# Kernel optimization log

Measured on AMD Instinct MI355X. Metric: run time of the kernel, lower is better.

The kernel has to match this reference:

```python
import jax, jax.numpy as jnp
import numpy as np

K_NEIGHBORS = 32  # nsample

def setup_inputs() -> dict:
    key = jax.random.key(0)
    ks = jax.random.split(key, 16)
    B, C, N = 4, 3, 4096
    def w(k, shape):
        return jax.random.normal(k, shape, dtype=jnp.float32) * 0.05
    inp = {"x": jax.random.normal(ks[0], (B, C, N), dtype=jnp.float32)}
    # three scale MLPs share shapes -> stack along leading scale axis (s=3)
    inp["sW0"] = w(ks[1], (3, 64, 3));    inp["sb0"] = w(ks[2], (3, 64))
    inp["sW1"] = w(ks[3], (3, 64, 64));   inp["sb1"] = w(ks[4], (3, 64))
    inp["sW2"] = w(ks[5], (3, 128, 64));  inp["sb2"] = w(ks[6], (3, 128))
    inp["gW0"] = w(ks[7], (256, 384));    inp["gb0"] = w(ks[8], (256,))
    inp["gW1"] = w(ks[9], (1024, 256));   inp["gb1"] = w(ks[10], (1024,))
    inp["mW0"] = w(ks[11], (256, 1024));  inp["mb0"] = w(ks[12], (256,))
    inp["mW1"] = w(ks[13], (128, 256));   inp["mb1"] = w(ks[14], (128,))
    return inp

def _knn_idx(x, k):
    # x: [B, 3, N] channels-first points; k nearest neighbors excluding self
    pts = jnp.swapaxes(x, 1, 2)                       # [B, N, 3]
    sq = jnp.sum(pts * pts, axis=-1)                  # [B, N]
    d = sq[:, :, None] + sq[:, None, :] - 2.0 * jnp.einsum('bnc,bmc->bnm', pts, pts)
    _, idx = jax.lax.top_k(-d, k + 1)                 # nearest first (self at 0)
    return idx[:, :, 1:]                              # [B, N, k]

def reference(x, sW0, sb0, sW1, sb1, sW2, sb2, gW0, gb0, gW1, gb1, mW0, mb0, mW1, mb1):
    B, C, N = x.shape
    # radius is unused by sample_and_group_knn -> all three scales share knn idx
    idx = _knn_idx(x, K_NEIGHBORS)                    # [B, N, K]
    # gather: per-batch x[:, idx[b]] -> [B, C, N, K]
    g = jax.vmap(lambda xf, i: xf[:, i])(x, idx)
    # three shared-weight 1x1-conv MLPs, batched over scale axis s
    h = jax.nn.relu(jnp.einsum('bcnk,soc->sbonk', g, sW0) + sb0[:, None, :, None, None])
    h = jax.nn.relu(jnp.einsum('sbcnk,soc->sbonk', h, sW1) + sb1[:, None, :, None, None])
    h = jax.nn.relu(jnp.einsum('sbcnk,soc->sbonk', h, sW2) + sb2[:, None, :, None, None])
    p = jnp.max(h, axis=-1)                           # [3, B, 128, N] max over neighbors
    point = jnp.moveaxis(p, 0, 1).reshape(B, 3 * p.shape[2], N)  # concat scales -> [B, 384, N]
    gf = jax.nn.relu(jnp.einsum('bcn,oc->bon', point, gW0) + gb0[None, :, None])
    gf = jax.nn.relu(jnp.einsum('bcn,oc->bon', gf, gW1) + gb1[None, :, None])     # [B,1024,N]
    msf = jax.nn.relu(jnp.einsum('bcn,oc->bon', gf, mW0) + mb0[None, :, None])
    msf = jax.nn.relu(jnp.einsum('bcn,oc->bon', msf, mW1) + mb1[None, :, None])   # [B,128,N]
    global_feature = jnp.max(gf, axis=-1)             # [B, 1024]
    return (global_feature, msf)
```

## Files before the change

### kernel.cpp

```cpp
#include <hip/hip_runtime.h>
#include <hip/hip_bf16.h>

#define NPTS 4096
#define KNN  32

typedef __attribute__((ext_vector_type(8))) short short8;
typedef __attribute__((ext_vector_type(4))) float floatx4;
typedef unsigned short u16x2 __attribute__((ext_vector_type(2)));

__device__ __forceinline__ unsigned short f2bf(float f) {
    unsigned u = __float_as_uint(f);
    u = (u + 0x7FFFu + ((u >> 16) & 1u)) >> 16;
    return (unsigned short)u;
}

__global__ __launch_bounds__(256) void prep_all(
    const float* __restrict__ x, float4* __restrict__ pts4,
    const float* __restrict__ gW0, const float* __restrict__ gW1,
    const float* __restrict__ mW0, const float* __restrict__ mW1,
    const float* __restrict__ sW1, const float* __restrict__ sW2,
    unsigned short* __restrict__ Wb0, unsigned short* __restrict__ Wb1,
    unsigned short* __restrict__ Wb2, unsigned short* __restrict__ Wb3,
    unsigned short* __restrict__ Wb4, unsigned short* __restrict__ Wb5)
{
    const int blk = blockIdx.x, t = threadIdx.x;
    if (blk < 64) {
        const int i = blk * 256 + t;
        const int b = i >> 12, n = i & (NPTS - 1);
        const float* xb = x + (size_t)b * 3 * NPTS;
        const float qx = xb[n], qy = xb[NPTS + n], qz = xb[2 * NPTS + n];
        pts4[i] = make_float4(qx, qy, qz, qx * qx + qy * qy + qz * qz);
    } else {
        const int wi = (blk - 64) * 256 + t;
        float v; unsigned short* dst;
        if (wi < 98304)       { v = gW0[wi];          dst = Wb0 + wi; }
        else if (wi < 360448) { v = gW1[wi - 98304];  dst = Wb1 + (wi - 98304); }
        else if (wi < 622592) { v = mW0[wi - 360448]; dst = Wb2 + (wi - 360448); }
        else if (wi < 655360) { v = mW1[wi - 622592]; dst = Wb3 + (wi - 622592); }
        else if (wi < 667648) { v = sW1[wi - 655360]; dst = Wb4 + (wi - 655360); }
        else                  { v = sW2[wi - 667648]; dst = Wb5 + (wi - 667648); }
        *dst = f2bf(v);
    }
}

__global__ __launch_bounds__(256) void knn_kernel16(const float4* __restrict__ pts4,
                                                    int* __restrict__ knn_out)
{
    __shared__ unsigned sred[2][4];
    __shared__ unsigned minS[256];
    __shared__ unsigned long long C[256];
    __shared__ unsigned ccnt;

    const int t = threadIdx.x, wid = t >> 6, lane = t & 63;
    const int q = blockIdx.x, b = q >> 12, n = q & (NPTS - 1);
    const float4* P = pts4 + ((size_t)b << 12);
    const float4 s = P[n];
    const float px = s.x, py = s.y, pz = s.z, sqn = s.w;

    if (t == 0) ccnt = 0u;

    unsigned key[16];
    #pragma unroll
    for (int g = 0; g < 4; ++g) {
        float4 c0 = P[((g * 4 + 0) << 8) + t];
        float4 c1 = P[((g * 4 + 1) << 8) + t];
        float4 c2 = P[((g * 4 + 2) << 8) + t];
        float4 c3 = P[((g * 4 + 3) << 8) + t];
        float d0 = (sqn + c0.w) - 2.0f * (px * c0.x + py * c0.y + pz * c0.z);
        float d1 = (sqn + c1.w) - 2.0f * (px * c1.x + py * c1.y + pz * c1.z);
        float d2 = (sqn + c2.w) - 2.0f * (px * c2.x + py * c2.y + pz * c2.z);
        float d3 = (sqn + c3.w) - 2.0f * (px * c3.x + py * c3.y + pz * c3.z);
        unsigned u0 = __float_as_uint(d0), u1 = __float_as_uint(d1);
        unsigned u2 = __float_as_uint(d2), u3 = __float_as_uint(d3);
        key[g * 4 + 0] = (u0 & 0x80000000u) ? ~u0 : (u0 | 0x80000000u);
        key[g * 4 + 1] = (u1 & 0x80000000u) ? ~u1 : (u1 | 0x80000000u);
        key[g * 4 + 2] = (u2 & 0x80000000u) ? ~u2 : (u2 | 0x80000000u);
        key[g * 4 + 3] = (u3 & 0x80000000u) ? ~u3 : (u3 | 0x80000000u);
    }

    unsigned tm = key[0];
    #pragma unroll
    for (int r = 1; r < 16; ++r) tm = (key[r] < tm) ? key[r] : tm;
    minS[t] = tm;
    __syncthreads();

    unsigned m0 = minS[lane];
    unsigned m1 = minS[lane + 64];
    unsigned m2 = minS[lane + 128];
    unsigned m3 = minS[lane + 192];
    m0 = (m1 < m0) ? m1 : m0;
    m2 = (m3 < m2) ? m3 : m2;
    m0 = (m2 < m0) ? m2 : m0;

    unsigned lo = 0u, hi = 0xFFFFFFFFu;
    for (int i = 0; i < 32; ++i) {
        const unsigned mid = lo + ((hi - lo) >> 1);
        const unsigned cnt = (unsigned)__popcll(__ballot(m0 <= mid));
        if (cnt >= 33u) hi = mid; else lo = mid + 1u;
    }
    const unsigned thr0 = hi;

    #pragma unroll
    for (int r = 0; r < 16; ++r) {
        if (key[r] <= thr0) {
            unsigned p = atomicAdd(&ccnt, 1u);
            if (p < 256u)
                C[p] = ((unsigned long long)key[r] << 32) |
                       (unsigned)((r << 8) + t);
        }
    }
    __syncthreads();

    int nc = (int)ccnt;
    if (nc > 256) {
        if (t == 0) ccnt = 0u;
        int pp = 0;
        auto countLE = [&](unsigned thr) -> unsigned {
            unsigned c = 0;
            #pragma unroll
            for (int r = 0; r < 16; ++r)
                c += (unsigned)__popcll(__ballot(key[r] <= thr));
            if (lane == 0) sred[pp & 1][wid] = c;
            __syncthreads();
            const unsigned g = sred[pp & 1][0] + sred[pp & 1][1] +
                               sred[pp & 1][2] + sred[pp & 1][3];
            ++pp;
            return g;
        };
        unsigned lo2 = 0x100u, hi2 = 0x1FEu, cntHi = 4096u;
        for (int it = 0; it < 8; ++it) {
            const unsigned mid = (lo2 + hi2) >> 1;
            const unsigned g = countLE((mid << 23) | 0x7FFFFFu);
            if (g >= 33u) { hi2 = mid; cntHi = g; } else lo2 = mid + 1u;
        }
        unsigned loK = lo2 << 23;
        unsigned hiK = (lo2 << 23) | 0x7FFFFFu;
        unsigned cntF = cntHi;
        while (cntF > 256u && loK < hiK) {
            const unsigned midK = loK + ((hiK - loK) >> 1);
            const unsigned c = countLE(midK);
            if (c >= 33u) { hiK = midK; cntF = c; } else loK = midK + 1u;
        }
        const unsigned thrF = hiK;
        #pragma unroll
        for (int r = 0; r < 16; ++r) {
            if (key[r] <= thrF) {
                unsigned p = atomicAdd(&ccnt, 1u);
                if (p < 256u)
                    C[p] = ((unsigned long long)key[r] << 32) |
                           (unsigned)((r << 8) + t);
            }
        }
        __syncthreads();
        nc = (int)ccnt; if (nc > 256) nc = 256;
    }

    if (t < nc) {
        const unsigned long long me = C[t];
        int rank = 0;
        for (int j = 0; j < nc; ++j) rank += (C[j] < me) ? 1 : 0;
        if (rank >= 1 && rank <= KNN)
            knn_out[(size_t)q * KNN + (rank - 1)] = (int)(me & 0xFFFFFFFFu);
    }
}

__global__ __launch_bounds__(256) void pointmlp_mfma(
    const float* __restrict__ x,
    const float* __restrict__ sW0, const float* __restrict__ sb0,
    const unsigned short* __restrict__ W1b, const float* __restrict__ sb1,
    const unsigned short* __restrict__ W2b, const float* __restrict__ sb2,
    unsigned short* __restrict__ F)
{
    __shared__ __align__(16) unsigned short W1s[64 * 72];
    __shared__ __align__(16) unsigned short W2s[128 * 72];
    __shared__ __align__(16) unsigned short h0T[32 * 72];
    __shared__ __align__(16) unsigned short h1T[32 * 72];
    __shared__ float W0s[192];
    __shared__ float b0s[64], b1s[64], b2s[128];
    __shared__ float pts[3 * 33];

    const int t = threadIdx.x;
    const int s = blockIdx.y;
    const int tile = blockIdx.x;
    const int b = tile >> 7;
    const int j0 = (tile & 127) << 5;
    const float* xb = x + (size_t)b * 3 * NPTS;

    if (t < 192) W0s[t] = sW0[s * 192 + t];
    if (t < 64) b0s[t] = sb0[s * 64 + t];
    if (t >= 64 && t < 128) b1s[t - 64] = sb1[s * 64 + (t - 64)];
    if (t < 128) b2s[t] = sb2[s * 128 + t];
    if (t < 96) { int c = t >> 5, p = t & 31; pts[c * 33 + p] = xb[c * NPTS + j0 + p]; }
    {
        const int o = t & 63, qq = t >> 6;
        const unsigned short* src = W1b + (size_t)s * 4096 + o * 64 + qq * 16;
        *(uint4*)&W1s[o * 72 + qq * 16]     = *(const uint4*)src;
        *(uint4*)&W1s[o * 72 + qq * 16 + 8] = *(const uint4*)(src + 8);
    }
    {
        const int o2 = t & 127, hh = t >> 7;
        const unsigned short* src = W2b + (size_t)s * 8192 + o2 * 64 + hh * 32;
        *(uint4*)&W2s[o2 * 72 + hh * 32]      = *(const uint4*)src;
        *(uint4*)&W2s[o2 * 72 + hh * 32 + 8]  = *(const uint4*)(src + 8);
        *(uint4*)&W2s[o2 * 72 + hh * 32 + 16] = *(const uint4*)(src + 16);
        *(uint4*)&W2s[o2 * 72 + hh * 32 + 24] = *(const uint4*)(src + 24);
    }
    __syncthreads();

    {
        const int p = t & 31, og = t >> 5;
        const float xx = pts[p], yy = pts[33 + p], zz = pts[66 + p];
        unsigned short hv[8];
        #pragma unroll
        for (int r = 0; r < 8; ++r) {
            const int o = og * 8 + r;
            float a = b0s[o] + W0s[o * 3] * xx + W0s[o * 3 + 1] * yy
                    + W0s[o * 3 + 2] * zz;
            hv[r] = f2bf(fmaxf(a, 0.0f));
        }
        *(uint4*)&h0T[p * 72 + og * 8] = *(const uint4*)hv;
    }
    __syncthreads();

    const int w = t >> 6, lane = t & 63, quad = lane >> 4, l15 = lane & 15;

    {
        #pragma unroll
        for (int ni = 0; ni < 2; ++ni) {
            floatx4 acc = (floatx4){0.f, 0.f, 0.f, 0.f};
            #pragma unroll
            for (int k0 = 0; k0 < 2; ++k0) {
                short8 aF = *(const short8*)&W1s[(w * 16 + l15) * 72 + k0 * 32 + quad * 8];
                short8 bF = *(const short8*)&h0T[(ni * 16 + l15) * 72 + k0 * 32 + quad * 8];
                acc = __builtin_amdgcn_mfma_f32_16x16x32_bf16(aF, bF, acc, 0, 0, 0);
            }
            const int m0 = w * 16 + quad * 4;
            const int p = ni * 16 + l15;
            ushort4 pk;
            pk.x = f2bf(fmaxf(acc[0] + b1s[m0 + 0], 0.f));
            pk.y = f2bf(fmaxf(acc[1] + b1s[m0 + 1], 0.f));
            pk.z = f2bf(fmaxf(acc[2] + b1s[m0 + 2], 0.f));
            pk.w = f2bf(fmaxf(acc[3] + b1s[m0 + 3], 0.f));
            *(ushort4*)&h1T[p * 72 + m0] = pk;
        }
    }
    __syncthreads();

    {
        #pragma unroll
        for (int mi = 0; mi < 2; ++mi) {
            const int m0 = (w * 2 + mi) * 16;
            #pragma unroll
            for (int ni = 0; ni < 2; ++ni) {
                floatx4 acc = (floatx4){0.f, 0.f, 0.f, 0.f};
                #pragma unroll
                for (int k0 = 0; k0 < 2; ++k0) {
                    short8 aF = *(const short8*)&W2s[(m0 + l15) * 72 + k0 * 32 + quad * 8];
                    short8 bF = *(const short8*)&h1T[(ni * 16 + l15) * 72 + k0 * 32 + quad * 8];
                    acc = __builtin_amdgcn_mfma_f32_16x16x32_bf16(aF, bF, acc, 0, 0, 0);
                }
                const int o2 = m0 + quad * 4;
                const int j = j0 + ni * 16 + l15;
                ushort4 pk;
                pk.x = f2bf(fmaxf(acc[0] + b2s[o2 + 0], 0.f));
                pk.y = f2bf(fmaxf(acc[1] + b2s[o2 + 1], 0.f));
                pk.z = f2bf(fmaxf(acc[2] + b2s[o2 + 2], 0.f));
                pk.w = f2bf(fmaxf(acc[3] + b2s[o2 + 3], 0.f));
                *(ushort4*)&F[((size_t)b * NPTS + j) * 384 + s * 128 + o2] = pk;
            }
        }
    }
}

__global__ __launch_bounds__(192) void maxgather_bf16(
    const unsigned short* __restrict__ F, const int* __restrict__ knn,
    unsigned short* __restrict__ pt)
{
    __shared__ int idxS[KNN];
    const int q = blockIdx.x;
    const int b = q >> 12;
    const int t = threadIdx.x;
    if (t < KNN) idxS[t] = knn[(size_t)q * KNN + t];
    __syncthreads();
    const unsigned short* Fb = F + (size_t)b * NPTS * 384 + t * 2;
    u16x2 m = (u16x2)0;
    #pragma unroll 8
    for (int k = 0; k < KNN; ++k) {
        u16x2 v = *(const u16x2*)(Fb + (size_t)idxS[k] * 384);
        m = __builtin_elementwise_max(m, v);
    }
    *(u16x2*)(pt + (size_t)q * 384 + t * 2) = m;
}

template<int DO_ROWMAX>
__global__ __launch_bounds__(256) void gemm_bf16(
    const unsigned short* __restrict__ Wb, const unsigned short* __restrict__ Bt,
    const float* __restrict__ bias, void* __restrict__ outp,
    float* __restrict__ gfeat, int M, int K)
{
    __shared__ __align__(16) unsigned short As[128 * 40];
    __shared__ __align__(16) unsigned short Bs[128 * 40];
    __shared__ float biasS[128];
    __shared__ int redI[128];

    const int t = threadIdx.x;
    const int b = blockIdx.z;
    const int m0 = blockIdx.x * 128;
    const int n0 = blockIdx.y * 128;
    if (t < 128) biasS[t] = bias[m0 + t];
    if (DO_ROWMAX && t < 128) redI[t] = 0;

    const int wave = t >> 6, lane = t & 63, quad = lane >> 4, l15 = lane & 15;
    const int wr = wave >> 1, wc = wave & 1;

    const int am = t & 127, akh = t >> 7;
    const unsigned short* Wp = Wb + (size_t)(m0 + am) * K + akh * 16;
    const int bn = t >> 2, bq = t & 3;
    const unsigned short* Bp = Bt + ((size_t)b * NPTS + n0) * K;

    floatx4 acc[16];
    #pragma unroll
    for (int i = 0; i < 16; ++i) acc[i] = (floatx4){0.f, 0.f, 0.f, 0.f};

    const int nk = K >> 5;
    for (int kt = 0; kt < nk; ++kt) {
        const int k0 = kt << 5;
        uint4 av0 = *(const uint4*)(Wp + k0);
        uint4 av1 = *(const uint4*)(Wp + k0 + 8);
        uint4 bv0 = *(const uint4*)(Bp + (size_t)bn * K + k0 + bq * 8);
        uint4 bv1 = *(const uint4*)(Bp + (size_t)(bn + 64) * K + k0 + bq * 8);
        __syncthreads();
        {
            uint4* dst = (uint4*)&As[am * 40 + akh * 16];
            dst[0] = av0;
            dst[1] = av1;
            *(uint4*)&Bs[bn * 40 + bq * 8] = bv0;
            *(uint4*)&Bs[(bn + 64) * 40 + bq * 8] = bv1;
        }
        __syncthreads();
        short8 af[4], bfv[4];
        #pragma unroll
        for (int i = 0; i < 4; ++i)
            af[i] = *(const short8*)&As[(wr * 64 + i * 16 + l15) * 40 + quad * 8];
        #pragma unroll
        for (int j = 0; j < 4; ++j)
            bfv[j] = *(const short8*)&Bs[(wc * 64 + j * 16 + l15) * 40 + quad * 8];
        #pragma unroll
        for (int i = 0; i < 4; ++i)
            #pragma unroll
            for (int j = 0; j < 4; ++j)
                acc[i * 4 + j] = __builtin_amdgcn_mfma_f32_16x16x32_bf16(
                    af[i], bfv[j], acc[i * 4 + j], 0, 0, 0);
    }

    #pragma unroll
    for (int i = 0; i < 4; ++i) {
        const int mbase = wr * 64 + i * 16 + quad * 4;
        float rm0 = 0.f, rm1 = 0.f, rm2 = 0.f, rm3 = 0.f;
        #pragma unroll
        for (int j = 0; j < 4; ++j) {
            const int n = n0 + wc * 64 + j * 16 + l15;
            float v0 = fmaxf(acc[i * 4 + j][0] + biasS[mbase + 0], 0.f);
            float v1 = fmaxf(acc[i * 4 + j][1] + biasS[mbase + 1], 0.f);
            float v2 = fmaxf(acc[i * 4 + j][2] + biasS[mbase + 2], 0.f);
            float v3 = fmaxf(acc[i * 4 + j][3] + biasS[mbase + 3], 0.f);
            if (DO_ROWMAX) {
                rm0 = fmaxf(rm0, v0); rm1 = fmaxf(rm1, v1);
                rm2 = fmaxf(rm2, v2); rm3 = fmaxf(rm3, v3);
            }
            ushort4 pk;
            pk.x = f2bf(v0); pk.y = f2bf(v1); pk.z = f2bf(v2); pk.w = f2bf(v3);
            *(ushort4*)((unsigned short*)outp +
                        ((size_t)b * NPTS + n) * M + m0 + mbase) = pk;
        }
        if (DO_ROWMAX) {
            atomicMax(&redI[mbase + 0], __float_as_int(rm0));
            atomicMax(&redI[mbase + 1], __float_as_int(rm1));
            atomicMax(&redI[mbase + 2], __float_as_int(rm2));
            atomicMax(&redI[mbase + 3], __float_as_int(rm3));
        }
    }
    if (DO_ROWMAX) {
        __syncthreads();
        if (t < 128)
            atomicMax((int*)&gfeat[(size_t)b * 1024 + m0 + t], redI[t]);
    }
}

__global__ __launch_bounds__(256) void fused_head(
    const unsigned short* __restrict__ Wb2, const unsigned short* __restrict__ Wb3,
    const float* __restrict__ mb0, const float* __restrict__ mb1,
    const unsigned short* __restrict__ gft, float* __restrict__ outp)
{
    __shared__ __align__(16) unsigned short As[256 * 40];
    __shared__ __align__(16) unsigned short Bs[64 * 40];
    __shared__ __align__(16) unsigned short H[64 * 264];
    __shared__ float b0s[256];
    __shared__ float b1s[128];

    const int t = threadIdx.x;
    const int n0 = blockIdx.x * 64;
    const int b = blockIdx.y;
    b0s[t] = mb0[t];
    if (t < 128) b1s[t] = mb1[t];

    const int wave = t >> 6, lane = t & 63, quad = lane >> 4, l15 = lane & 15;

    const unsigned short* Ap = Wb2 + (size_t)t * 1024;
    const int bn = t >> 2, bq = t & 3;
    const unsigned short* Bp = gft + ((size_t)b * NPTS + n0) * 1024;

    floatx4 acc[16];
    #pragma unroll
    for (int i = 0; i < 16; ++i) acc[i] = (floatx4){0.f, 0.f, 0.f, 0.f};

    for (int kt = 0; kt < 32; ++kt) {
        const int k0 = kt << 5;
        uint4 a0 = *(const uint4*)(Ap + k0);
        uint4 a1 = *(const uint4*)(Ap + k0 + 8);
        uint4 a2 = *(const uint4*)(Ap + k0 + 16);
        uint4 a3 = *(const uint4*)(Ap + k0 + 24);
        uint4 bv = *(const uint4*)(Bp + (size_t)bn * 1024 + k0 + bq * 8);
        __syncthreads();
        *(uint4*)&As[t * 40 + 0]  = a0;
        *(uint4*)&As[t * 40 + 8]  = a1;
        *(uint4*)&As[t * 40 + 16] = a2;
        *(uint4*)&As[t * 40 + 24] = a3;
        *(uint4*)&Bs[bn * 40 + bq * 8] = bv;
        __syncthreads();
        short8 af[4], bfv[4];
        #pragma unroll
        for (int i = 0; i < 4; ++i)
            af[i] = *(const short8*)&As[(wave * 64 + i * 16 + l15) * 40 + quad * 8];
        #pragma unroll
        for (int j = 0; j < 4; ++j)
            bfv[j] = *(const short8*)&Bs[(j * 16 + l15) * 40 + quad * 8];
        #pragma unroll
        for (int i = 0; i < 4; ++i)
            #pragma unroll
            for (int j = 0; j < 4; ++j)
                acc[i * 4 + j] = __builtin_amdgcn_mfma_f32_16x16x32_bf16(
                    af[i], bfv[j], acc[i * 4 + j], 0, 0, 0);
    }
    #pragma unroll
    for (int i = 0; i < 4; ++i) {
        const int mbase = wave * 64 + i * 16 + quad * 4;
        #pragma unroll
        for (int j = 0; j < 4; ++j) {
            const int nl = j * 16 + l15;
            ushort4 pk;
            pk.x = f2bf(fmaxf(acc[i * 4 + j][0] + b0s[mbase + 0], 0.f));
            pk.y = f2bf(fmaxf(acc[i * 4 + j][1] + b0s[mbase + 1], 0.f));
            pk.z = f2bf(fmaxf(acc[i * 4 + j][2] + b0s[mbase + 2], 0.f));
            pk.w = f2bf(fmaxf(acc[i * 4 + j][3] + b0s[mbase + 3], 0.f));
            *(ushort4*)&H[nl * 264 + mbase] = pk;
        }
    }

    floatx4 acc2[8];
    #pragma unroll
    for (int i = 0; i < 8; ++i) acc2[i] = (floatx4){0.f, 0.f, 0.f, 0.f};
    const int am2 = t & 127, ah = t >> 7;

    for (int kt = 0; kt < 8; ++kt) {
        const int k0 = kt << 5;
        uint4 a0 = *(const uint4*)(Wb3 + (size_t)am2 * 256 + k0 + ah * 16);
        uint4 a1 = *(const uint4*)(Wb3 + (size_t)am2 * 256 + k0 + ah * 16 + 8);
        __syncthreads();
        *(uint4*)&As[am2 * 40 + ah * 16]     = a0;
        *(uint4*)&As[am2 * 40 + ah * 16 + 8] = a1;
        __syncthreads();
        short8 af2[2], bf2[4];
        #pragma unroll
        for (int i = 0; i < 2; ++i)
            af2[i] = *(const short8*)&As[(wave * 32 + i * 16 + l15) * 40 + quad * 8];
        #pragma unroll
        for (int j = 0; j < 4; ++j)
            bf2[j] = *(const short8*)&H[(j * 16 + l15) * 264 + k0 + quad * 8];
        #pragma unroll
        for (int i = 0; i < 2; ++i)
            #pragma unroll
            for (int j = 0; j < 4; ++j)
                acc2[i * 4 + j] = __builtin_amdgcn_mfma_f32_16x16x32_bf16(
                    af2[i], bf2[j], acc2[i * 4 + j], 0, 0, 0);
    }
    #pragma unroll
    for (int i = 0; i < 2; ++i) {
        const int m2 = wave * 32 + i * 16 + quad * 4;
        #pragma unroll
        for (int j = 0; j < 4; ++j) {
            const int n = n0 + j * 16 + l15;
            float* o = outp + ((size_t)b * 128 + m2) * NPTS + n;
            o[0 * NPTS] = fmaxf(acc2[i * 4 + j][0] + b1s[m2 + 0], 0.f);
            o[1 * NPTS] = fmaxf(acc2[i * 4 + j][1] + b1s[m2 + 1], 0.f);
            o[2 * NPTS] = fmaxf(acc2[i * 4 + j][2] + b1s[m2 + 2], 0.f);
            o[3 * NPTS] = fmaxf(acc2[i * 4 + j][3] + b1s[m2 + 3], 0.f);
        }
    }
}

extern "C" void kernel_launch(void* const* d_in, const int* in_sizes, int n_in,
                              void* d_out, int out_size, void* d_ws, size_t ws_size,
                              hipStream_t stream)
{
    const float* x   = (const float*)d_in[0];
    const float* sW0 = (const float*)d_in[1];
    const float* sb0 = (const float*)d_in[2];
    const float* sW1 = (const float*)d_in[3];
    const float* sb1 = (const float*)d_in[4];
    const float* sW2 = (const float*)d_in[5];
    const float* sb2 = (const float*)d_in[6];
    const float* gW0 = (const float*)d_in[7];
    const float* gb0 = (const float*)d_in[8];
    const float* gW1 = (const float*)d_in[9];
    const float* gb1 = (const float*)d_in[10];
    const float* mW0 = (const float*)d_in[11];
    const float* mb0 = (const float*)d_in[12];
    const float* mW1 = (const float*)d_in[13];
    const float* mb1 = (const float*)d_in[14];
    float* outp = (float*)d_out;

    char* ws = (char*)d_ws;
    int*            idx     = (int*)(ws);
    float4*         pts4    = (float4*)(ws + 2097152u);
    unsigned short* Wb0     = (unsigned short*)(ws + 2359296u);
    unsigned short* Wb1     = (unsigned short*)(ws + 2555904u);
    unsigned short* Wb2     = (unsigned short*)(ws + 3080192u);
    unsigned short* Wb3     = (unsigned short*)(ws + 3604480u);
    unsigned short* Wb4     = (unsigned short*)(ws + 3670016u);
    unsigned short* Wb5     = (unsigned short*)(ws + 3694592u);
    unsigned short* F       = (unsigned short*)(ws + 4194304u);
    unsigned short* point_t = (unsigned short*)(ws + 18874368u);
    unsigned short* gf0t    = (unsigned short*)(ws + 33554432u);
    unsigned short* gft     = (unsigned short*)(ws + 50331648u);

    prep_all<<<dim3(2768), dim3(256), 0, stream>>>(
        x, pts4, gW0, gW1, mW0, mW1, sW1, sW2, Wb0, Wb1, Wb2, Wb3, Wb4, Wb5);
    knn_kernel16<<<dim3(16384), dim3(256), 0, stream>>>(pts4, idx);
    pointmlp_mfma<<<dim3(512, 3), dim3(256), 0, stream>>>(
        x, sW0, sb0, Wb4, sb1, Wb5, sb2, F);
    maxgather_bf16<<<dim3(16384), dim3(192), 0, stream>>>(F, idx, point_t);
    gemm_bf16<0><<<dim3(2, 32, 4), dim3(256), 0, stream>>>(
        Wb0, point_t, gb0, gf0t, nullptr, 256, 384);
    gemm_bf16<1><<<dim3(8, 32, 4), dim3(256), 0, stream>>>(
        Wb1, gf0t, gb1, gft, outp, 1024, 256);
    fused_head<<<dim3(64, 4), dim3(256), 0, stream>>>(
        Wb2, Wb3, mb0, mb1, gft, outp + 4096);
}
```

Baseline: 250.8 us.

## Shorten kNN threshold search, unroll rank step, widen gW1 GEMM tile to 256

The kNN kernel now binary-searches the candidate threshold on the top 16 bits of the sortable key, which halves the ballot loop. It computes keys with branchless XOR. When at most 64 candidates survive, it ranks them with a fixed unrolled 64-entry loop over sentinel-padded shared memory. A new GEMM variant with a 128x256 tile replaces the 1024x256 layer GEMM, halving the grid and reusing each weight tile across more points, at the cost of 32 accumulator registers per thread and possibly lower occupancy. The coarser threshold may admit more candidates and push more queries onto the slower fallback path.

```diff
diff --git a/kernel.cpp b/kernel.cpp
--- a/kernel.cpp
+++ b/kernel.cpp
@@ -43,7 +43,7 @@
     }
 }
 
-__global__ __launch_bounds__(256) void knn_kernel16(const float4* __restrict__ pts4,
+__global__ __launch_bounds__(256) void knn_kernel17(const float4* __restrict__ pts4,
                                                     int* __restrict__ knn_out)
 {
     __shared__ unsigned sred[2][4];
@@ -58,6 +58,7 @@
     const float px = s.x, py = s.y, pz = s.z, sqn = s.w;
 
     if (t == 0) ccnt = 0u;
+    C[t] = 0xFFFFFFFFFFFFFFFFULL;
 
     unsigned key[16];
     #pragma unroll
@@ -72,10 +73,10 @@
         float d3 = (sqn + c3.w) - 2.0f * (px * c3.x + py * c3.y + pz * c3.z);
         unsigned u0 = __float_as_uint(d0), u1 = __float_as_uint(d1);
         unsigned u2 = __float_as_uint(d2), u3 = __float_as_uint(d3);
-        key[g * 4 + 0] = (u0 & 0x80000000u) ? ~u0 : (u0 | 0x80000000u);
-        key[g * 4 + 1] = (u1 & 0x80000000u) ? ~u1 : (u1 | 0x80000000u);
-        key[g * 4 + 2] = (u2 & 0x80000000u) ? ~u2 : (u2 | 0x80000000u);
-        key[g * 4 + 3] = (u3 & 0x80000000u) ? ~u3 : (u3 | 0x80000000u);
+        key[g * 4 + 0] = u0 ^ (((unsigned)((int)u0 >> 31)) | 0x80000000u);
+        key[g * 4 + 1] = u1 ^ (((unsigned)((int)u1 >> 31)) | 0x80000000u);
+        key[g * 4 + 2] = u2 ^ (((unsigned)((int)u2 >> 31)) | 0x80000000u);
+        key[g * 4 + 3] = u3 ^ (((unsigned)((int)u3 >> 31)) | 0x80000000u);
     }
 
     unsigned tm = key[0];
@@ -92,13 +93,14 @@
     m2 = (m3 < m2) ? m3 : m2;
     m0 = (m2 < m0) ? m2 : m0;
 
-    unsigned lo = 0u, hi = 0xFFFFFFFFu;
-    for (int i = 0; i < 32; ++i) {
-        const unsigned mid = lo + ((hi - lo) >> 1);
-        const unsigned cnt = (unsigned)__popcll(__ballot(m0 <= mid));
+    const unsigned ms16 = m0 >> 16;
+    unsigned lo = 0u, hi = 0xFFFFu;
+    for (int i = 0; i < 16; ++i) {
+        const unsigned mid = (lo + hi) >> 1;
+        const unsigned cnt = (unsigned)__popcll(__ballot(ms16 <= mid));
         if (cnt >= 33u) hi = mid; else lo = mid + 1u;
     }
-    const unsigned thr0 = hi;
+    const unsigned thr0 = (hi << 16) | 0xFFFFu;
 
     #pragma unroll
     for (int r = 0; r < 16; ++r) {
@@ -112,7 +114,9 @@
     __syncthreads();
 
     int nc = (int)ccnt;
+    bool fell_back = false;
     if (nc > 256) {
+        fell_back = true;
         if (t == 0) ccnt = 0u;
         int pp = 0;
         auto countLE = [&](unsigned thr) -> unsigned {
@@ -155,12 +159,23 @@
         nc = (int)ccnt; if (nc > 256) nc = 256;
     }
 
-    if (t < nc) {
-        const unsigned long long me = C[t];
-        int rank = 0;
-        for (int j = 0; j < nc; ++j) rank += (C[j] < me) ? 1 : 0;
-        if (rank >= 1 && rank <= KNN)
-            knn_out[(size_t)q * KNN + (rank - 1)] = (int)(me & 0xFFFFFFFFu);
+    if (!fell_back && nc <= 64) {
+        if (t < 64) {
+            const unsigned long long me = C[t];
+            int rank = 0;
+            #pragma unroll
+            for (int j = 0; j < 64; ++j) rank += (C[j] < me) ? 1 : 0;
+            if (rank >= 1 && rank <= KNN)
+                knn_out[(size_t)q * KNN + (rank - 1)] = (int)(me & 0xFFFFFFFFu);
+        }
+    } else {
+        if (t < nc) {
+            const unsigned long long me = C[t];
+            int rank = 0;
+            for (int j = 0; j < nc; ++j) rank += (C[j] < me) ? 1 : 0;
+            if (rank >= 1 && rank <= KNN)
+                knn_out[(size_t)q * KNN + (rank - 1)] = (int)(me & 0xFFFFFFFFu);
+        }
     }
 }
 
@@ -387,6 +402,105 @@
     }
 }
 
+template<int DO_ROWMAX>
+__global__ __launch_bounds__(256) void gemm_bf16_n256(
+    const unsigned short* __restrict__ Wb, const unsigned short* __restrict__ Bt,
+    const float* __restrict__ bias, void* __restrict__ outp,
+    float* __restrict__ gfeat, int M, int K)
+{
+    __shared__ __align__(16) unsigned short As[128 * 40];
+    __shared__ __align__(16) unsigned short Bs[256 * 40];
+    __shared__ float biasS[128];
+    __shared__ int redI[128];
+
+    const int t = threadIdx.x;
+    const int b = blockIdx.z;
+    const int m0 = blockIdx.x * 128;
+    const int n0 = blockIdx.y * 256;
+    if (t < 128) biasS[t] = bias[m0 + t];
+    if (DO_ROWMAX && t < 128) redI[t] = 0;
+
+    const int wave = t >> 6, lane = t & 63, quad = lane >> 4, l15 = lane & 15;
+    const int wr = wave >> 1, wc = wave & 1;
+
+    const int am = t & 127, akh = t >> 7;
+    const unsigned short* Wp = Wb + (size_t)(m0 + am) * K + akh * 16;
+    const int bn = t >> 2, bq = t & 3;
+    const unsigned short* Bp = Bt + ((size_t)b * NPTS + n0) * K;
+
+    floatx4 acc[32];
+    #pragma unroll
+    for (int i = 0; i < 32; ++i) acc[i] = (floatx4){0.f, 0.f, 0.f, 0.f};
+
+    const int nk = K >> 5;
+    for (int kt = 0; kt < nk; ++kt) {
+        const int k0 = kt << 5;
+        uint4 av0 = *(const uint4*)(Wp + k0);
+        uint4 av1 = *(const uint4*)(Wp + k0 + 8);
+        uint4 bv0 = *(const uint4*)(Bp + (size_t)(bn +   0) * K + k0 + bq * 8);
+        uint4 bv1 = *(const uint4*)(Bp + (size_t)(bn +  64) * K + k0 + bq * 8);
+        uint4 bv2 = *(const uint4*)(Bp + (size_t)(bn + 128) * K + k0 + bq * 8);
+        uint4 bv3 = *(const uint4*)(Bp + (size_t)(bn + 192) * K + k0 + bq * 8);
+        __syncthreads();
+        {
+            uint4* dst = (uint4*)&As[am * 40 + akh * 16];
+            dst[0] = av0;
+            dst[1] = av1;
+            *(uint4*)&Bs[(bn +   0) * 40 + bq * 8] = bv0;
+            *(uint4*)&Bs[(bn +  64) * 40 + bq * 8] = bv1;
+            *(uint4*)&Bs[(bn + 128) * 40 + bq * 8] = bv2;
+            *(uint4*)&Bs[(bn + 192) * 40 + bq * 8] = bv3;
+        }
+        __syncthreads();
+        short8 af[4], bfv[8];
+        #pragma unroll
+        for (int i = 0; i < 4; ++i)
+            af[i] = *(const short8*)&As[(wr * 64 + i * 16 + l15) * 40 + quad * 8];
+        #pragma unroll
+        for (int j = 0; j < 8; ++j)
+            bfv[j] = *(const short8*)&Bs[(wc * 128 + j * 16 + l15) * 40 + quad * 8];
+        #pragma unroll
+        for (int i = 0; i < 4; ++i)
+            #pragma unroll
+            for (int j = 0; j < 8; ++j)
+                acc[i * 8 + j] = __builtin_amdgcn_mfma_f32_16x16x32_bf16(
+                    af[i], bfv[j], acc[i * 8 + j], 0, 0, 0);
+    }
+
+    #pragma unroll
+    for (int i = 0; i < 4; ++i) {
+        const int mbase = wr * 64 + i * 16 + quad * 4;
+        float rm0 = 0.f, rm1 = 0.f, rm2 = 0.f, rm3 = 0.f;
+        #pragma unroll
+        for (int j = 0; j < 8; ++j) {
+            const int n = n0 + wc * 128 + j * 16 + l15;
+            float v0 = fmaxf(acc[i * 8 + j][0] + biasS[mbase + 0], 0.f);
+            float v1 = fmaxf(acc[i * 8 + j][1] + biasS[mbase + 1], 0.f);
+            float v2 = fmaxf(acc[i * 8 + j][2] + biasS[mbase + 2], 0.f);
+            float v3 = fmaxf(acc[i * 8 + j][3] + biasS[mbase + 3], 0.f);
+            if (DO_ROWMAX) {
+                rm0 = fmaxf(rm0, v0); rm1 = fmaxf(rm1, v1);
+                rm2 = fmaxf(rm2, v2); rm3 = fmaxf(rm3, v3);
+            }
+            ushort4 pk;
+            pk.x = f2bf(v0); pk.y = f2bf(v1); pk.z = f2bf(v2); pk.w = f2bf(v3);
+            *(ushort4*)((unsigned short*)outp +
+                        ((size_t)b * NPTS + n) * M + m0 + mbase) = pk;
+        }
+        if (DO_ROWMAX) {
+            atomicMax(&redI[mbase + 0], __float_as_int(rm0));
+            atomicMax(&redI[mbase + 1], __float_as_int(rm1));
+            atomicMax(&redI[mbase + 2], __float_as_int(rm2));
+            atomicMax(&redI[mbase + 3], __float_as_int(rm3));
+        }
+    }
+    if (DO_ROWMAX) {
+        __syncthreads();
+        if (t < 128)
+            atomicMax((int*)&gfeat[(size_t)b * 1024 + m0 + t], redI[t]);
+    }
+}
+
 __global__ __launch_bounds__(256) void fused_head(
     const unsigned short* __restrict__ Wb2, const unsigned short* __restrict__ Wb3,
     const float* __restrict__ mb0, const float* __restrict__ mb1,
@@ -536,13 +650,13 @@
 
     prep_all<<<dim3(2768), dim3(256), 0, stream>>>(
         x, pts4, gW0, gW1, mW0, mW1, sW1, sW2, Wb0, Wb1, Wb2, Wb3, Wb4, Wb5);
-    knn_kernel16<<<dim3(16384), dim3(256), 0, stream>>>(pts4, idx);
+    knn_kernel17<<<dim3(16384), dim3(256), 0, stream>>>(pts4, idx);
     pointmlp_mfma<<<dim3(512, 3), dim3(256), 0, stream>>>(
         x, sW0, sb0, Wb4, sb1, Wb5, sb2, F);
     maxgather_bf16<<<dim3(16384), dim3(192), 0, stream>>>(F, idx, point_t);
     gemm_bf16<0><<<dim3(2, 32, 4), dim3(256), 0, stream>>>(
         Wb0, point_t, gb0, gf0t, nullptr, 256, 384);
-    gemm_bf16<1><<<dim3(8, 32, 4), dim3(256), 0, stream>>>(
+    gemm_bf16_n256<1><<<dim3(8, 16, 4), dim3(256), 0, stream>>>(
         Wb1, gf0t, gb1, gft, outp, 1024, 256);
     fused_head<<<dim3(64, 4), dim3(256), 0, stream>>>(
         Wb2, Wb3, mb0, mb1, gft, outp + 4096);
```

Measured after the change: 245.6 us. -2.1%, faster.

## Fuse kNN and per-point MLP into one heterogeneous kernel launch

Applied to the files above, without the earlier changes.

Merges the kNN selection kernel and the per-scale point MLP kernel into one launch. Blocks are interleaved so that of every 35 blocks, 3 run point-MLP tiles and 32 run kNN queries, all sharing one raw shared-memory buffer. This removes a launch boundary and lets the two independent stages run concurrently. The kNN path also gets a branchless float-to-key transform, a 16-step binary search on the upper 16 key bits instead of 32 steps, and a fixed 64-wide unrolled ranking when there are few candidates. The coarser threshold can admit more candidates, making the slow fallback more likely. The larger shared-memory footprint for kNN blocks may reduce occupancy.

```diff
diff --git a/kernel.cpp b/kernel.cpp
--- a/kernel.cpp
+++ b/kernel.cpp
@@ -43,21 +43,139 @@
     }
 }
 
-__global__ __launch_bounds__(256) void knn_kernel16(const float4* __restrict__ pts4,
-                                                    int* __restrict__ knn_out)
+__global__ __launch_bounds__(256) void knn_pointmlp_fused(
+    const float4* __restrict__ pts4, int* __restrict__ knn_out,
+    const float* __restrict__ x,
+    const float* __restrict__ sW0, const float* __restrict__ sb0,
+    const unsigned short* __restrict__ W1b, const float* __restrict__ sb1,
+    const unsigned short* __restrict__ W2b, const float* __restrict__ sb2,
+    unsigned short* __restrict__ F)
 {
-    __shared__ unsigned sred[2][4];
-    __shared__ unsigned minS[256];
-    __shared__ unsigned long long C[256];
-    __shared__ unsigned ccnt;
-
-    const int t = threadIdx.x, wid = t >> 6, lane = t & 63;
-    const int q = blockIdx.x, b = q >> 12, n = q & (NPTS - 1);
+    __shared__ __align__(16) char smem[39104];
+
+    const int t = threadIdx.x;
+    const int bid = blockIdx.x;
+    const int grp = bid / 35, rr = bid % 35;
+
+    if (rr < 3) {
+        const int pm_id = grp * 3 + rr;
+        unsigned short* W1s = (unsigned short*)(smem);
+        unsigned short* W2s = (unsigned short*)(smem + 9216);
+        unsigned short* h0T = (unsigned short*)(smem + 27648);
+        unsigned short* h1T = (unsigned short*)(smem + 32256);
+        float* W0s = (float*)(smem + 36864);
+        float* b0s = (float*)(smem + 37632);
+        float* b1s = (float*)(smem + 37888);
+        float* b2s = (float*)(smem + 38144);
+        float* pts = (float*)(smem + 38656);
+
+        const int s = pm_id / 512;
+        const int tile = pm_id % 512;
+        const int b = tile >> 7;
+        const int j0 = (tile & 127) << 5;
+        const float* xb = x + (size_t)b * 3 * NPTS;
+
+        if (t < 192) W0s[t] = sW0[s * 192 + t];
+        if (t < 64) b0s[t] = sb0[s * 64 + t];
+        if (t >= 64 && t < 128) b1s[t - 64] = sb1[s * 64 + (t - 64)];
+        if (t < 128) b2s[t] = sb2[s * 128 + t];
+        if (t < 96) { int c = t >> 5, p = t & 31; pts[c * 33 + p] = xb[c * NPTS + j0 + p]; }
+        {
+            const int o = t & 63, qq = t >> 6;
+            const unsigned short* src = W1b + (size_t)s * 4096 + o * 64 + qq * 16;
+            *(uint4*)&W1s[o * 72 + qq * 16]     = *(const uint4*)src;
+            *(uint4*)&W1s[o * 72 + qq * 16 + 8] = *(const uint4*)(src + 8);
+        }
+        {
+            const int o2 = t & 127, hh = t >> 7;
+            const unsigned short* src = W2b + (size_t)s * 8192 + o2 * 64 + hh * 32;
+            *(uint4*)&W2s[o2 * 72 + hh * 32]      = *(const uint4*)src;
+            *(uint4*)&W2s[o2 * 72 + hh * 32 + 8]  = *(const uint4*)(src + 8);
+            *(uint4*)&W2s[o2 * 72 + hh * 32 + 16] = *(const uint4*)(src + 16);
+            *(uint4*)&W2s[o2 * 72 + hh * 32 + 24] = *(const uint4*)(src + 24);
+        }
+        __syncthreads();
+
+        {
+            const int p = t & 31, og = t >> 5;
+            const float xx = pts[p], yy = pts[33 + p], zz = pts[66 + p];
+            unsigned short hv[8];
+            #pragma unroll
+            for (int r = 0; r < 8; ++r) {
+                const int o = og * 8 + r;
+                float a = b0s[o] + W0s[o * 3] * xx + W0s[o * 3 + 1] * yy
+                        + W0s[o * 3 + 2] * zz;
+                hv[r] = f2bf(fmaxf(a, 0.0f));
+            }
+            *(uint4*)&h0T[p * 72 + og * 8] = *(const uint4*)hv;
+        }
+        __syncthreads();
+
+        const int w = t >> 6, lane = t & 63, quad = lane >> 4, l15 = lane & 15;
+
+        {
+            #pragma unroll
+            for (int ni = 0; ni < 2; ++ni) {
+                floatx4 acc = (floatx4){0.f, 0.f, 0.f, 0.f};
+                #pragma unroll
+                for (int k0 = 0; k0 < 2; ++k0) {
+                    short8 aF = *(const short8*)&W1s[(w * 16 + l15) * 72 + k0 * 32 + quad * 8];
+                    short8 bF = *(const short8*)&h0T[(ni * 16 + l15) * 72 + k0 * 32 + quad * 8];
+                    acc = __builtin_amdgcn_mfma_f32_16x16x32_bf16(aF, bF, acc, 0, 0, 0);
+                }
+                const int m0 = w * 16 + quad * 4;
+                const int p = ni * 16 + l15;
+                ushort4 pk;
+                pk.x = f2bf(fmaxf(acc[0] + b1s[m0 + 0], 0.f));
+                pk.y = f2bf(fmaxf(acc[1] + b1s[m0 + 1], 0.f));
+                pk.z = f2bf(fmaxf(acc[2] + b1s[m0 + 2], 0.f));
+                pk.w = f2bf(fmaxf(acc[3] + b1s[m0 + 3], 0.f));
+                *(ushort4*)&h1T[p * 72 + m0] = pk;
+            }
+        }
+        __syncthreads();
+
+        {
+            #pragma unroll
+            for (int mi = 0; mi < 2; ++mi) {
+                const int m0 = (w * 2 + mi) * 16;
+                #pragma unroll
+                for (int ni = 0; ni < 2; ++ni) {
+                    floatx4 acc = (floatx4){0.f, 0.f, 0.f, 0.f};
+                    #pragma unroll
+                    for (int k0 = 0; k0 < 2; ++k0) {
+                        short8 aF = *(const short8*)&W2s[(m0 + l15) * 72 + k0 * 32 + quad * 8];
+                        short8 bF = *(const short8*)&h1T[(ni * 16 + l15) * 72 + k0 * 32 + quad * 8];
+                        acc = __builtin_amdgcn_mfma_f32_16x16x32_bf16(aF, bF, acc, 0, 0, 0);
+                    }
+                    const int o2 = m0 + quad * 4;
+                    const int j = j0 + ni * 16 + l15;
+                    ushort4 pk;
+                    pk.x = f2bf(fmaxf(acc[0] + b2s[o2 + 0], 0.f));
+                    pk.y = f2bf(fmaxf(acc[1] + b2s[o2 + 1], 0.f));
+                    pk.z = f2bf(fmaxf(acc[2] + b2s[o2 + 2], 0.f));
+                    pk.w = f2bf(fmaxf(acc[3] + b2s[o2 + 3], 0.f));
+                    *(ushort4*)&F[((size_t)b * NPTS + j) * 384 + s * 128 + o2] = pk;
+                }
+            }
+        }
+        return;
+    }
+
+    const int kq = grp * 32 + (rr - 3);
+    unsigned (*sred)[4]     = (unsigned(*)[4])(smem);
+    unsigned* minS          = (unsigned*)(smem + 32);
+    unsigned long long* C   = (unsigned long long*)(smem + 1056);
+    unsigned* ccntP         = (unsigned*)(smem + 3104);
+
+    const int wid = t >> 6, lane = t & 63;
+    const int q = kq, b = q >> 12, n = q & (NPTS - 1);
     const float4* P = pts4 + ((size_t)b << 12);
     const float4 s = P[n];
     const float px = s.x, py = s.y, pz = s.z, sqn = s.w;
 
-    if (t == 0) ccnt = 0u;
+    if (t == 0) *ccntP = 0u;
+    C[t] = 0xFFFFFFFFFFFFFFFFULL;
 
     unsigned key[16];
     #pragma unroll
@@ -72,10 +190,10 @@
         float d3 = (sqn + c3.w) - 2.0f * (px * c3.x + py * c3.y + pz * c3.z);
         unsigned u0 = __float_as_uint(d0), u1 = __float_as_uint(d1);
         unsigned u2 = __float_as_uint(d2), u3 = __float_as_uint(d3);
-        key[g * 4 + 0] = (u0 & 0x80000000u) ? ~u0 : (u0 | 0x80000000u);
-        key[g * 4 + 1] = (u1 & 0x80000000u) ? ~u1 : (u1 | 0x80000000u);
-        key[g * 4 + 2] = (u2 & 0x80000000u) ? ~u2 : (u2 | 0x80000000u);
-        key[g * 4 + 3] = (u3 & 0x80000000u) ? ~u3 : (u3 | 0x80000000u);
+        key[g * 4 + 0] = u0 ^ (((unsigned)((int)u0 >> 31)) | 0x80000000u);
+        key[g * 4 + 1] = u1 ^ (((unsigned)((int)u1 >> 31)) | 0x80000000u);
+        key[g * 4 + 2] = u2 ^ (((unsigned)((int)u2 >> 31)) | 0x80000000u);
+        key[g * 4 + 3] = u3 ^ (((unsigned)((int)u3 >> 31)) | 0x80000000u);
     }
 
     unsigned tm = key[0];
@@ -92,18 +210,19 @@
     m2 = (m3 < m2) ? m3 : m2;
     m0 = (m2 < m0) ? m2 : m0;
 
-    unsigned lo = 0u, hi = 0xFFFFFFFFu;
-    for (int i = 0; i < 32; ++i) {
-        const unsigned mid = lo + ((hi - lo) >> 1);
-        const unsigned cnt = (unsigned)__popcll(__ballot(m0 <= mid));
+    const unsigned ms16 = m0 >> 16;
+    unsigned lo = 0u, hi = 0xFFFFu;
+    for (int i = 0; i < 16; ++i) {
+        const unsigned mid = (lo + hi) >> 1;
+        const unsigned cnt = (unsigned)__popcll(__ballot(ms16 <= mid));
         if (cnt >= 33u) hi = mid; else lo = mid + 1u;
     }
-    const unsigned thr0 = hi;
+    const unsigned thr0 = (hi << 16) | 0xFFFFu;
 
     #pragma unroll
     for (int r = 0; r < 16; ++r) {
         if (key[r] <= thr0) {
-            unsigned p = atomicAdd(&ccnt, 1u);
+            unsigned p = atomicAdd(ccntP, 1u);
             if (p < 256u)
                 C[p] = ((unsigned long long)key[r] << 32) |
                        (unsigned)((r << 8) + t);
@@ -111,9 +230,11 @@
     }
     __syncthreads();
 
-    int nc = (int)ccnt;
+    int nc = (int)*ccntP;
+    bool fell_back = false;
     if (nc > 256) {
-        if (t == 0) ccnt = 0u;
+        fell_back = true;
+        if (t == 0) *ccntP = 0u;
         int pp = 0;
         auto countLE = [&](unsigned thr) -> unsigned {
             unsigned c = 0;
@@ -145,129 +266,32 @@
         #pragma unroll
         for (int r = 0; r < 16; ++r) {
             if (key[r] <= thrF) {
-                unsigned p = atomicAdd(&ccnt, 1u);
+                unsigned p = atomicAdd(ccntP, 1u);
                 if (p < 256u)
                     C[p] = ((unsigned long long)key[r] << 32) |
                            (unsigned)((r << 8) + t);
             }
         }
         __syncthreads();
-        nc = (int)ccnt; if (nc > 256) nc = 256;
-    }
-
-    if (t < nc) {
-        const unsigned long long me = C[t];
-        int rank = 0;
-        for (int j = 0; j < nc; ++j) rank += (C[j] < me) ? 1 : 0;
-        if (rank >= 1 && rank <= KNN)
-            knn_out[(size_t)q * KNN + (rank - 1)] = (int)(me & 0xFFFFFFFFu);
-    }
-}
-
-__global__ __launch_bounds__(256) void pointmlp_mfma(
-    const float* __restrict__ x,
-    const float* __restrict__ sW0, const float* __restrict__ sb0,
-    const unsigned short* __restrict__ W1b, const float* __restrict__ sb1,
-    const unsigned short* __restrict__ W2b, const float* __restrict__ sb2,
-    unsigned short* __restrict__ F)
-{
-    __shared__ __align__(16) unsigned short W1s[64 * 72];
-    __shared__ __align__(16) unsigned short W2s[128 * 72];
-    __shared__ __align__(16) unsigned short h0T[32 * 72];
-    __shared__ __align__(16) unsigned short h1T[32 * 72];
-    __shared__ float W0s[192];
-    __shared__ float b0s[64], b1s[64], b2s[128];
-    __shared__ float pts[3 * 33];
-
-    const int t = threadIdx.x;
-    const int s = blockIdx.y;
-    const int tile = blockIdx.x;
-    const int b = tile >> 7;
-    const int j0 = (tile & 127) << 5;
-    const float* xb = x + (size_t)b * 3 * NPTS;
-
-    if (t < 192) W0s[t] = sW0[s * 192 + t];
-    if (t < 64) b0s[t] = sb0[s * 64 + t];
-    if (t >= 64 && t < 128) b1s[t - 64] = sb1[s * 64 + (t - 64)];
-    if (t < 128) b2s[t] = sb2[s * 128 + t];
-    if (t < 96) { int c = t >> 5, p = t & 31; pts[c * 33 + p] = xb[c * NPTS + j0 + p]; }
-    {
-        const int o = t & 63, qq = t >> 6;
-        const unsigned short* src = W1b + (size_t)s * 4096 + o * 64 + qq * 16;
-        *(uint4*)&W1s[o * 72 + qq * 16]     = *(const uint4*)src;
-        *(uint4*)&W1s[o * 72 + qq * 16 + 8] = *(const uint4*)(src + 8);
-    }
-    {
-        const int o2 = t & 127, hh = t >> 7;
-        const unsigned short* src = W2b + (size_t)s * 8192 + o2 * 64 + hh * 32;
-        *(uint4*)&W2s[o2 * 72 + hh * 32]      = *(const uint4*)src;
-        *(uint4*)&W2s[o2 * 72 + hh * 32 + 8]  = *(const uint4*)(src + 8);
-        *(uint4*)&W2s[o2 * 72 + hh * 32 + 16] = *(const uint4*)(src + 16);
-        *(uint4*)&W2s[o2 * 72 + hh * 32 + 24] = *(const uint4*)(src + 24);
-    }
-    __syncthreads();
-
-    {
-        const int p = t & 31, og = t >> 5;
-        const float xx = pts[p], yy = pts[33 + p], zz = pts[66 + p];
-        unsigned short hv[8];
-        #pragma unroll
-        for (int r = 0; r < 8; ++r) {
-            const int o = og * 8 + r;
-            float a = b0s[o] + W0s[o * 3] * xx + W0s[o * 3 + 1] * yy
-                    + W0s[o * 3 + 2] * zz;
-            hv[r] = f2bf(fmaxf(a, 0.0f));
-        }
-        *(uint4*)&h0T[p * 72 + og * 8] = *(const uint4*)hv;
-    }
-    __syncthreads();
-
-    const int w = t >> 6, lane = t & 63, quad = lane >> 4, l15 = lane & 15;
-
-    {
-        #pragma unroll
-        for (int ni = 0; ni < 2; ++ni) {
-            floatx4 acc = (floatx4){0.f, 0.f, 0.f, 0.f};
-            #pragma unroll
-            for (int k0 = 0; k0 < 2; ++k0) {
-                short8 aF = *(const short8*)&W1s[(w * 16 + l15) * 72 + k0 * 32 + quad * 8];
-                short8 bF = *(const short8*)&h0T[(ni * 16 + l15) * 72 + k0 * 32 + quad * 8];
-                acc = __builtin_amdgcn_mfma_f32_16x16x32_bf16(aF, bF, acc, 0, 0, 0);
-            }
-            const int m0 = w * 16 + quad * 4;
-            const int p = ni * 16 + l15;
-            ushort4 pk;
-            pk.x = f2bf(fmaxf(acc[0] + b1s[m0 + 0], 0.f));
-            pk.y = f2bf(fmaxf(acc[1] + b1s[m0 + 1], 0.f));
-            pk.z = f2bf(fmaxf(acc[2] + b1s[m0 + 2], 0.f));
-            pk.w = f2bf(fmaxf(acc[3] + b1s[m0 + 3], 0.f));
-            *(ushort4*)&h1T[p * 72 + m0] = pk;
-        }
-    }
-    __syncthreads();
-
-    {
-        #pragma unroll
-        for (int mi = 0; mi < 2; ++mi) {
-            const int m0 = (w * 2 + mi) * 16;
-            #pragma unroll
-            for (int ni = 0; ni < 2; ++ni) {
-                floatx4 acc = (floatx4){0.f, 0.f, 0.f, 0.f};
-                #pragma unroll
-                for (int k0 = 0; k0 < 2; ++k0) {
-                    short8 aF = *(const short8*)&W2s[(m0 + l15) * 72 + k0 * 32 + quad * 8];
-                    short8 bF = *(const short8*)&h1T[(ni * 16 + l15) * 72 + k0 * 32 + quad * 8];
-                    acc = __builtin_amdgcn_mfma_f32_16x16x32_bf16(aF, bF, acc, 0, 0, 0);
-                }
-                const int o2 = m0 + quad * 4;
-                const int j = j0 + ni * 16 + l15;
-                ushort4 pk;
-                pk.x = f2bf(fmaxf(acc[0] + b2s[o2 + 0], 0.f));
-                pk.y = f2bf(fmaxf(acc[1] + b2s[o2 + 1], 0.f));
-                pk.z = f2bf(fmaxf(acc[2] + b2s[o2 + 2], 0.f));
-                pk.w = f2bf(fmaxf(acc[3] + b2s[o2 + 3], 0.f));
-                *(ushort4*)&F[((size_t)b * NPTS + j) * 384 + s * 128 + o2] = pk;
-            }
+        nc = (int)*ccntP; if (nc > 256) nc = 256;
+    }
+
+    if (!fell_back && nc <= 64) {
+        if (t < 64) {
+            const unsigned long long me = C[t];
+            int rank = 0;
+            #pragma unroll
+            for (int j = 0; j < 64; ++j) rank += (C[j] < me) ? 1 : 0;
+            if (rank >= 1 && rank <= KNN)
+                knn_out[(size_t)q * KNN + (rank - 1)] = (int)(me & 0xFFFFFFFFu);
+        }
+    } else {
+        if (t < nc) {
+            const unsigned long long me = C[t];
+            int rank = 0;
+            for (int j = 0; j < nc; ++j) rank += (C[j] < me) ? 1 : 0;
+            if (rank >= 1 && rank <= KNN)
+                knn_out[(size_t)q * KNN + (rank - 1)] = (int)(me & 0xFFFFFFFFu);
         }
     }
 }
@@ -536,9 +560,8 @@
 
     prep_all<<<dim3(2768), dim3(256), 0, stream>>>(
         x, pts4, gW0, gW1, mW0, mW1, sW1, sW2, Wb0, Wb1, Wb2, Wb3, Wb4, Wb5);
-    knn_kernel16<<<dim3(16384), dim3(256), 0, stream>>>(pts4, idx);
-    pointmlp_mfma<<<dim3(512, 3), dim3(256), 0, stream>>>(
-        x, sW0, sb0, Wb4, sb1, Wb5, sb2, F);
+    knn_pointmlp_fused<<<dim3(17920), dim3(256), 0, stream>>>(
+        pts4, idx, x, sW0, sb0, Wb4, sb1, Wb5, sb2, F);
     maxgather_bf16<<<dim3(16384), dim3(192), 0, stream>>>(F, idx, point_t);
     gemm_bf16<0><<<dim3(2, 32, 4), dim3(256), 0, stream>>>(
         Wb0, point_t, gb0, gf0t, nullptr, 256, 384);
```

New measurement: 259.3 us. 1.03x slower.
